# Kernel optimization log

Hardware: AMD Instinct MI355X
Metric: run time of the kernel (lower is better)

The kernel has to match this reference:

```python
import jax, jax.numpy as jnp
import numpy as np

T, B, H = 2048, 32, 1024


def setup_inputs() -> dict:
    key = jax.random.key(0)
    k1, k2, k3 = jax.random.split(key, 3)
    t_input = jax.random.normal(k1, (T, B, H), dtype=jnp.float32)
    h0 = jax.random.normal(k2, (B, H), dtype=jnp.float32)
    # weight_hh ~ U(0, 1) per reset_parameters default
    weight_hh = jax.random.uniform(k3, (H,), dtype=jnp.float32)
    return {"t_input": t_input, "h0": h0, "weight_hh": weight_hh}


def reference(t_input, h0, weight_hh):
    # h_t = relu(x_t + whh * h_{t-1}); per-channel recurrent scan over time.
    def step(h, x):
        h_new = jax.nn.relu(x + weight_hh * h)  # (B, H)
        return h_new, h_new

    _, out = jax.lax.scan(step, h0, t_input)  # out: (T, B, H)
    return out
```

## Files before the change

kernel.cpp:

```cpp
#include <hip/hip_runtime.h>


#define T_STEPS 2048
#define B_DIM   32
#define H_DIM   1024
#define BH      (B_DIM * H_DIM)
#define BH2     (BH / 2)
#define PF      32

typedef float f2 __attribute__((ext_vector_type(2)));

__global__ __launch_bounds__(64, 1)
void indrnn_kernel(const f2* __restrict__ x,
                   const f2* __restrict__ h0,
                   const f2* __restrict__ w,
                   f2* __restrict__ out)
{
    const int c2 = blockIdx.x * 64 + threadIdx.x;
    const f2 wv = w[c2 & (H_DIM / 2 - 1)];
    f2 h = h0[c2];

    const f2* xp = x + c2;
    f2* op = out + c2;

    f2 buf[PF];
#pragma unroll
    for (int i = 0; i < PF; ++i)
        buf[i] = __builtin_nontemporal_load(&xp[(size_t)i * BH2]);

    int t0 = 0;
    for (; t0 + PF < T_STEPS; t0 += PF) {
        f2 nxt[PF];
        const int tn = t0 + PF;
#pragma unroll
        for (int i = 0; i < PF; ++i)
            nxt[i] = __builtin_nontemporal_load(&xp[(size_t)(tn + i) * BH2]);

#pragma unroll
        for (int i = 0; i < PF; ++i) {
            h.x = fmaxf(fmaf(wv.x, h.x, buf[i].x), 0.0f);
            h.y = fmaxf(fmaf(wv.y, h.y, buf[i].y), 0.0f);
            __builtin_nontemporal_store(h, &op[(size_t)(t0 + i) * BH2]);
        }

#pragma unroll
        for (int i = 0; i < PF; ++i)
            buf[i] = nxt[i];
    }

#pragma unroll
    for (int i = 0; i < PF; ++i) {
        h.x = fmaxf(fmaf(wv.x, h.x, buf[i].x), 0.0f);
        h.y = fmaxf(fmaf(wv.y, h.y, buf[i].y), 0.0f);
        __builtin_nontemporal_store(h, &op[(size_t)(t0 + i) * BH2]);
    }
}

extern "C" void kernel_launch(void* const* d_in, const int* in_sizes, int n_in,
                              void* d_out, int out_size, void* d_ws, size_t ws_size,
                              hipStream_t stream) {
    const f2* x  = (const f2*)d_in[0];
    const f2* h0 = (const f2*)d_in[1];
    const f2* w  = (const f2*)d_in[2];
    f2* out = (f2*)d_out;

    indrnn_kernel<<<BH2 / 64, 64, 0, stream>>>(x, h0, w, out);
}
```

Baseline: 421.1 us.

## Split the time scan into chunks with a three-pass composed-recurrence approach

Replaces the single long serial scan per channel with a chunked three-pass scheme. Pass 1 reduces each of 32 time chunks to a (max, affine) summary. Pass 2 composes the summaries with h = max(w^64*h + a, m) to get each chunk's starting state. Pass 3 reruns every chunk in parallel and writes the outputs. The aim is to expose far more parallelism than the 512 waves that were each serial over 2048 steps, which left the kernel latency-bound. The cost is reading the input twice plus workspace traffic. The composition rule relies on nonnegative weights, which holds for the uniform [0,1) init.

After: 480.7 us. +14.1%, slower.

```diff
diff --git a/kernel.cpp b/kernel.cpp
--- a/kernel.cpp
+++ b/kernel.cpp
@@ -6,22 +6,31 @@
 #define H_DIM   1024
 #define BH      (B_DIM * H_DIM)
 #define BH2     (BH / 2)
-#define PF      32
+#define NCHUNK  32
+#define CLEN    (T_STEPS / NCHUNK)
+#define PF      16
 
 typedef float f2 __attribute__((ext_vector_type(2)));
 
-__global__ __launch_bounds__(64, 1)
-void indrnn_kernel(const f2* __restrict__ x,
-                   const f2* __restrict__ h0,
-                   const f2* __restrict__ w,
-                   f2* __restrict__ out)
+__global__ __launch_bounds__(256, 4)
+void indrnn_pass1(const f2* __restrict__ x, const f2* __restrict__ h0,
+                  const f2* __restrict__ w,
+                  f2* __restrict__ m_out, f2* __restrict__ a_out)
 {
-    const int c2 = blockIdx.x * 64 + threadIdx.x;
+    const int tid = blockIdx.x * 256 + threadIdx.x;
+    const int c   = tid >> 14;
+    const int c2  = tid & (BH2 - 1);
     const f2 wv = w[c2 & (H_DIM / 2 - 1)];
-    f2 h = h0[c2];
 
-    const f2* xp = x + c2;
-    f2* op = out + c2;
+    f2 m, a;
+    a.x = 0.f; a.y = 0.f;
+    if (c == 0) {
+        m = h0[c2];
+    } else {
+        m.x = 0.f; m.y = 0.f;
+    }
+
+    const f2* xp = x + (size_t)c * CLEN * BH2 + c2;
 
     f2 buf[PF];
 #pragma unroll
@@ -29,25 +38,96 @@
         buf[i] = __builtin_nontemporal_load(&xp[(size_t)i * BH2]);
 
     int t0 = 0;
-    for (; t0 + PF < T_STEPS; t0 += PF) {
+    for (; t0 + PF < CLEN; t0 += PF) {
         f2 nxt[PF];
-        const int tn = t0 + PF;
 #pragma unroll
         for (int i = 0; i < PF; ++i)
-            nxt[i] = __builtin_nontemporal_load(&xp[(size_t)(tn + i) * BH2]);
+            nxt[i] = __builtin_nontemporal_load(&xp[(size_t)(t0 + PF + i) * BH2]);
+#pragma unroll
+        for (int i = 0; i < PF; ++i) {
+            m.x = fmaxf(fmaf(wv.x, m.x, buf[i].x), 0.f);
+            m.y = fmaxf(fmaf(wv.y, m.y, buf[i].y), 0.f);
+            a.x = fmaf(wv.x, a.x, buf[i].x);
+            a.y = fmaf(wv.y, a.y, buf[i].y);
+        }
+#pragma unroll
+        for (int i = 0; i < PF; ++i) buf[i] = nxt[i];
+    }
+#pragma unroll
+    for (int i = 0; i < PF; ++i) {
+        m.x = fmaxf(fmaf(wv.x, m.x, buf[i].x), 0.f);
+        m.y = fmaxf(fmaf(wv.y, m.y, buf[i].y), 0.f);
+        a.x = fmaf(wv.x, a.x, buf[i].x);
+        a.y = fmaf(wv.y, a.y, buf[i].y);
+    }
 
+    m_out[(size_t)c * BH2 + c2] = m;
+    a_out[(size_t)c * BH2 + c2] = a;
+}
+
+__global__ __launch_bounds__(256, 1)
+void indrnn_pass2(const float* __restrict__ h0, const float* __restrict__ w,
+                  const float* __restrict__ m, const float* __restrict__ a,
+                  float* __restrict__ hstart)
+{
+    const int ch = blockIdx.x * 256 + threadIdx.x;
+    const float wv = w[ch & (H_DIM - 1)];
+    float b = wv;
+#pragma unroll
+    for (int i = 0; i < 6; ++i) b *= b;
+
+    float mv[NCHUNK], av[NCHUNK];
+#pragma unroll
+    for (int cc = 0; cc < NCHUNK; ++cc) {
+        mv[cc] = m[cc * BH + ch];
+        av[cc] = a[cc * BH + ch];
+    }
+
+    float h = h0[ch];
+    hstart[ch] = h;
+    h = mv[0];
+    hstart[BH + ch] = h;
+#pragma unroll
+    for (int cc = 2; cc < NCHUNK; ++cc) {
+        h = fmaxf(fmaf(b, h, av[cc - 1]), mv[cc - 1]);
+        hstart[cc * BH + ch] = h;
+    }
+}
+
+__global__ __launch_bounds__(256, 4)
+void indrnn_pass3(const f2* __restrict__ x, const f2* __restrict__ hstart,
+                  const f2* __restrict__ w, f2* __restrict__ out)
+{
+    const int tid = blockIdx.x * 256 + threadIdx.x;
+    const int c   = tid >> 14;
+    const int c2  = tid & (BH2 - 1);
+    const f2 wv = w[c2 & (H_DIM / 2 - 1)];
+
+    f2 h = hstart[(size_t)c * BH2 + c2];
+
+    const f2* xp = x + (size_t)c * CLEN * BH2 + c2;
+    f2* op = out + (size_t)c * CLEN * BH2 + c2;
+
+    f2 buf[PF];
+#pragma unroll
+    for (int i = 0; i < PF; ++i)
+        buf[i] = __builtin_nontemporal_load(&xp[(size_t)i * BH2]);
+
+    int t0 = 0;
+    for (; t0 + PF < CLEN; t0 += PF) {
+        f2 nxt[PF];
+#pragma unroll
+        for (int i = 0; i < PF; ++i)
+            nxt[i] = __builtin_nontemporal_load(&xp[(size_t)(t0 + PF + i) * BH2]);
 #pragma unroll
         for (int i = 0; i < PF; ++i) {
             h.x = fmaxf(fmaf(wv.x, h.x, buf[i].x), 0.0f);
             h.y = fmaxf(fmaf(wv.y, h.y, buf[i].y), 0.0f);
             __builtin_nontemporal_store(h, &op[(size_t)(t0 + i) * BH2]);
         }
-
 #pragma unroll
-        for (int i = 0; i < PF; ++i)
-            buf[i] = nxt[i];
+        for (int i = 0; i < PF; ++i) buf[i] = nxt[i];
     }
-
 #pragma unroll
     for (int i = 0; i < PF; ++i) {
         h.x = fmaxf(fmaf(wv.x, h.x, buf[i].x), 0.0f);
@@ -64,5 +144,14 @@
     const f2* w  = (const f2*)d_in[2];
     f2* out = (f2*)d_out;
 
-    indrnn_kernel<<<BH2 / 64, 64, 0, stream>>>(x, h0, w, out);
+    float* m  = (float*)d_ws;
+    float* a  = m + (size_t)NCHUNK * BH;
+    float* hs = a + (size_t)NCHUNK * BH;
+
+    indrnn_pass1<<<(NCHUNK * BH2) / 256, 256, 0, stream>>>(
+        x, h0, w, (f2*)m, (f2*)a);
+    indrnn_pass2<<<BH / 256, 256, 0, stream>>>(
+        (const float*)h0, (const float*)w, m, a, hs);
+    indrnn_pass3<<<(NCHUNK * BH2) / 256, 256, 0, stream>>>(
+        x, (const f2*)hs, w, out);
 }
```
